# Optimization experiments

Measured on AMD Instinct MI355X. Metric: run time of the kernel, lower is better.

Reference implementation:

```python
import jax, jax.numpy as jnp
import numpy as np

DIM = 512
NUM_HEADS = 16
WS = 8  # window_size
N = WS * WS
B = 1024


def get_relative_index(h, w):
    coords_h = np.arange(h)[:, None].repeat(w, axis=1)
    coords_w = np.arange(w)[None, :].repeat(h, axis=0)
    coords = np.stack([coords_h, coords_w], axis=-1).reshape(-1, 2)  # [N,2]
    rel = coords[:, None, :] - coords[None, :, :]
    rel = rel + np.array([h - 1, w - 1])
    rel[:, :, 0] *= 2 * w - 1
    return rel.sum(-1).astype(np.int32)  # [N,N]


def setup_inputs() -> dict:
    key = jax.random.key(0)
    ks = jax.random.split(key, 6)
    table_size = (2 * WS - 1) * (2 * WS - 1)  # 225
    return {
        "x": jax.random.normal(ks[0], (B, N, DIM), dtype=jnp.float32),
        "qkv_weight": jax.random.normal(ks[1], (3 * DIM, DIM), dtype=jnp.float32) * 0.02,
        "qkv_bias": jax.random.normal(ks[2], (3 * DIM,), dtype=jnp.float32) * 0.02,
        "proj_weight": jax.random.normal(ks[3], (DIM, DIM), dtype=jnp.float32) * 0.02,
        "proj_bias": jax.random.normal(ks[4], (DIM,), dtype=jnp.float32) * 0.02,
        "relative_table": jax.random.normal(ks[5], (table_size, 2 * NUM_HEADS), dtype=jnp.float32) * 0.02,
        "relative_index": jnp.asarray(get_relative_index(WS, WS)),
    }


def reference(x, qkv_weight, qkv_bias, proj_weight, proj_bias, relative_table, relative_index):
    B_, n, C = x.shape
    H = NUM_HEADS
    hd = C // H
    scale = hd ** -0.5
    # qkv projection: [B,N,3C] -> [3,B,H,N,hd]
    qkv = (x @ qkv_weight.T + qkv_bias).reshape(B_, n, 3, H, hd).transpose(2, 0, 3, 1, 4)
    q, k, v = qkv[0], qkv[1], qkv[2]
    attn = jnp.einsum("bhnd,bhmd->bhnm", q * scale, k)  # [B,H,N,N]
    # learned relative-position bias + post-softmax scale
    params = relative_table[relative_index.reshape(-1)].reshape(n, n, 2 * H)
    params = params.transpose(2, 0, 1)  # [2H,N,N]
    rel_bias, rel_scale = params[:H], params[H:]
    attn = jax.nn.softmax(attn + rel_bias[None], axis=-1)
    attn = attn * rel_scale[None]
    out = jnp.einsum("bhnm,bhmd->bhnd", attn, v)
    out = out.transpose(0, 2, 1, 3).reshape(B_, n, C)
    return out @ proj_weight.T + proj_bias
```

## Files before the change

kernel.cpp:

```cpp
#include <hip/hip_runtime.h>

typedef unsigned short u16;
typedef unsigned int   u32;
typedef __attribute__((ext_vector_type(8))) short bf16x8;
typedef __attribute__((ext_vector_type(4))) float f32x4;

#define SCALE 0.17677669529663687f

__device__ __forceinline__ u16 f2bf(float f){
  u32 x = __float_as_uint(f);
  x += 0x7fffu + ((x >> 16) & 1u);
  return (u16)(x >> 16);
}
__device__ __forceinline__ float bf2f(u16 u){
  return __uint_as_float(((u32)u) << 16);
}


__global__ void prep_kernel(const float* __restrict__ qkvw, const float* __restrict__ projw,
                            const float* __restrict__ table, const int* __restrict__ relidx,
                            u16* __restrict__ qkvw_b, u16* __restrict__ projw_b,
                            u16* __restrict__ biasT, u16* __restrict__ scaleT){
  int i = blockIdx.x * 256 + threadIdx.x;
  if (i < 786432) {
    qkvw_b[i] = f2bf(qkvw[i]);
  } else if (i < 1048576) {
    int j = i - 786432; projw_b[j] = f2bf(projw[j]);
  } else if (i < 1114112) {
    int j = i - 1048576; int h = j >> 12, rc = j & 4095;
    int idx = relidx[rc];
    biasT [h*4096 + rc] = f2bf(table[idx*32 + h]);
    scaleT[h*4096 + rc] = f2bf(table[idx*32 + 16 + h]);
  }
}

__global__ void xconv_kernel(const float* __restrict__ x, u16* __restrict__ xb){
  size_t i = (size_t)blockIdx.x * 256 + threadIdx.x;
  const float4* xp = (const float4*)x;
  float4 a = xp[2*i], b = xp[2*i+1];
  union { u16 u[8]; uint4 v; } o;
  o.u[0]=f2bf(a.x); o.u[1]=f2bf(a.y); o.u[2]=f2bf(a.z); o.u[3]=f2bf(a.w);
  o.u[4]=f2bf(b.x); o.u[5]=f2bf(b.y); o.u[6]=f2bf(b.z); o.u[7]=f2bf(b.w);
  *(uint4*)(xb + 8*i) = o.v;
}

template<int EPI>
__global__ __launch_bounds__(512, 2) void gemm_kernel(
    const u16* __restrict__ A, const u16* __restrict__ W,
    const float* __restrict__ bias, void* __restrict__ outp, const int NT)
{
  __shared__ u16 lds[3][16384];
  const int tid = threadIdx.x, lane = tid & 63, wid = tid >> 6;
  const int wave_base = tid & ~63;

  const int cpx = gridDim.x >> 3;
  const int bid = (blockIdx.x & 7) * cpx + (blockIdx.x >> 3);
  const int mt = bid / NT, nt = bid % NT;
  const size_t m0 = (size_t)mt * 256;
  const int n0 = nt * 256;
  const int wm = wid >> 2, wn = wid & 3;

  const f32x4 z = {0.f, 0.f, 0.f, 0.f};
  f32x4 acc[8][4];
#pragma unroll
  for (int i = 0; i < 8; i++)
#pragma unroll
    for (int j = 0; j < 4; j++) acc[i][j] = z;

  auto stageA = [&](int ch){
    const int slot = ch % 3;
    const int kb = ch * 32;
#pragma unroll
    for (int c = 0; c < 2; ++c){
      const int t = c*512 + tid;
      const int row = t >> 2, sl = t & 3;
      const int lsl = sl ^ ((row >> 1) & 3);
      const u16* ga = A + (m0 + row)*512 + kb + lsl*8;
      u16* la = &lds[slot][(size_t)(c*512 + wave_base)*8];
      __builtin_amdgcn_global_load_lds((const __attribute__((address_space(1))) u32*)ga,
                                       (__attribute__((address_space(3))) u32*)la, 16, 0, 0);
    }
  };
  auto stageB = [&](int ch){
    const int slot = ch % 3;
    const int kb = ch * 32;
#pragma unroll
    for (int c = 0; c < 2; ++c){
      const int t = c*512 + tid;
      const int col = t >> 2, sl = t & 3;
      const int lsl = sl ^ ((col >> 1) & 3);
      const u16* gb = W + (size_t)(n0 + col)*512 + kb + lsl*8;
      u16* lb = &lds[slot][8192 + (size_t)(c*512 + wave_base)*8];
      __builtin_amdgcn_global_load_lds((const __attribute__((address_space(1))) u32*)gb,
                                       (__attribute__((address_space(3))) u32*)lb, 16, 0, 0);
    }
  };

  stageA(0); stageB(0);
  stageA(1); stageB(1);
  asm volatile("s_waitcnt vmcnt(4)" ::: "memory");
  __builtin_amdgcn_s_barrier();

  const int lq = lane & 15, lk = lane >> 4;
#pragma unroll
  for (int ch = 0; ch < 16; ++ch){
    const int slot = ch % 3;
    const u16* As = &lds[slot][0];
    const u16* Bs = &lds[slot][8192];
    bf16x8 af[4], bfr[4], af2[4];

#pragma unroll
    for (int i = 0; i < 4; ++i){
      const int row = wm*128 + i*16 + lq;
      af[i]  = *(const bf16x8*)&As[row*32 + (lk ^ ((row >> 1) & 3))*8];
      const int col = wn*64 + i*16 + lq;
      bfr[i] = *(const bf16x8*)&Bs[col*32 + (lk ^ ((col >> 1) & 3))*8];
    }
    if (ch + 2 < 16) stageA(ch + 2);
    __builtin_amdgcn_s_barrier();
    asm volatile("s_waitcnt lgkmcnt(0)" ::: "memory");
    __builtin_amdgcn_sched_barrier(0);
    __builtin_amdgcn_s_setprio(1);
#pragma unroll
    for (int i = 0; i < 4; ++i)
#pragma unroll
      for (int j = 0; j < 4; ++j)
        acc[i][j] = __builtin_amdgcn_mfma_f32_16x16x32_bf16(af[i], bfr[j], acc[i][j], 0, 0, 0);
    __builtin_amdgcn_s_setprio(0);
    __builtin_amdgcn_s_barrier();

#pragma unroll
    for (int i = 0; i < 4; ++i){
      const int row = wm*128 + 64 + i*16 + lq;
      af2[i] = *(const bf16x8*)&As[row*32 + (lk ^ ((row >> 1) & 3))*8];
    }
    if (ch + 2 < 16) stageB(ch + 2);
    __builtin_amdgcn_s_barrier();
    asm volatile("s_waitcnt lgkmcnt(0)" ::: "memory");
    __builtin_amdgcn_sched_barrier(0);
    __builtin_amdgcn_s_setprio(1);
#pragma unroll
    for (int i = 0; i < 4; ++i)
#pragma unroll
      for (int j = 0; j < 4; ++j)
        acc[4+i][j] = __builtin_amdgcn_mfma_f32_16x16x32_bf16(af2[i], bfr[j], acc[4+i][j], 0, 0, 0);
    __builtin_amdgcn_s_setprio(0);
    if (ch < 14)       { asm volatile("s_waitcnt vmcnt(4)" ::: "memory"); }
    else if (ch == 14) { asm volatile("s_waitcnt vmcnt(0)" ::: "memory"); }
    if (ch < 15) __builtin_amdgcn_s_barrier();
  }

  const int lr = (lane >> 4) << 2;
  const int lc = lane & 15;
  if (EPI == 0){
    u16* o = (u16*)outp;
    float bv[4], sc[4];
#pragma unroll
    for (int nf = 0; nf < 4; ++nf){
      const int col = n0 + wn*64 + nf*16 + lc;
      bv[nf] = bias[col];
      sc[nf] = (col < 512) ? SCALE : 1.f;
    }
#pragma unroll
    for (int mf = 0; mf < 8; ++mf){
#pragma unroll
      for (int r = 0; r < 4; ++r){
        const size_t row = m0 + wm*128 + mf*16 + lr + r;
#pragma unroll
        for (int nf = 0; nf < 4; ++nf){
          const int col = n0 + wn*64 + nf*16 + lc;
          o[row*1536 + col] = f2bf((acc[mf][nf][r] + bv[nf]) * sc[nf]);
        }
      }
    }
  } else {
    float* o = (float*)outp;
    float bv[4];
#pragma unroll
    for (int nf = 0; nf < 4; ++nf)
      bv[nf] = bias[n0 + wn*64 + nf*16 + lc];
#pragma unroll
    for (int mf = 0; mf < 8; ++mf){
#pragma unroll
      for (int r = 0; r < 4; ++r){
        const size_t row = m0 + wm*128 + mf*16 + lr + r;
#pragma unroll
        for (int nf = 0; nf < 4; ++nf){
          const int col = n0 + wn*64 + nf*16 + lc;
          o[row*512 + col] = acc[mf][nf][r] + bv[nf];
        }
      }
    }
  }
}

__global__ __launch_bounds__(256) void attn_kernel(
    const u16* __restrict__ qkv, const u16* __restrict__ biasT,
    const u16* __restrict__ scaleT, u16* __restrict__ attn_out)
{
  __shared__ u16 qs[64*40];
  __shared__ u16 ks[64*40];
  __shared__ u16 vs[64*40];
  __shared__ u16 Ps[64*72];
  const int tid = threadIdx.x, lane = tid & 63, wid = tid >> 6;
  const int bh = blockIdx.x, b = bh >> 4, h = bh & 15;
  const u16* base = qkv + (size_t)b * 64 * 1536 + h * 32;
  {
    const int row = tid >> 2, seg = (tid & 3) * 8;
    const size_t ro = (size_t)row * 1536 + seg;
    *(uint4*)&qs[row*40 + seg] = *(const uint4*)(base + ro);
    *(uint4*)&ks[row*40 + seg] = *(const uint4*)(base + ro + 512);
    *(uint4*)&vs[row*40 + seg] = *(const uint4*)(base + ro + 1024);
  }
  __syncthreads();

  const int wr0 = wid * 16;
  const int lg = lane >> 4, lc = lane & 15;
  const f32x4 z = {0.f, 0.f, 0.f, 0.f};

  bf16x8 qf = *(const bf16x8*)&qs[(wr0 + lc)*40 + lg*8];
  f32x4 s[4];
#pragma unroll
  for (int ct = 0; ct < 4; ++ct){
    bf16x8 kf = *(const bf16x8*)&ks[(ct*16 + lc)*40 + lg*8];
    s[ct] = __builtin_amdgcn_mfma_f32_16x16x32_bf16(qf, kf, z, 0, 0, 0);
  }

  const u16* bT = biasT + h*4096;
  const u16* sT = scaleT + h*4096;
#pragma unroll
  for (int r = 0; r < 4; ++r){
    const int row = wr0 + lg*4 + r;
    float vals[4]; float mx = -1e30f;
#pragma unroll
    for (int ct = 0; ct < 4; ++ct){
      vals[ct] = s[ct][r] + bf2f(bT[row*64 + ct*16 + lc]);
      mx = fmaxf(mx, vals[ct]);
    }
    mx = fmaxf(mx, __shfl_xor(mx, 1));
    mx = fmaxf(mx, __shfl_xor(mx, 2));
    mx = fmaxf(mx, __shfl_xor(mx, 4));
    mx = fmaxf(mx, __shfl_xor(mx, 8));
    float sm = 0.f;
#pragma unroll
    for (int ct = 0; ct < 4; ++ct){ vals[ct] = __expf(vals[ct] - mx); sm += vals[ct]; }
    sm += __shfl_xor(sm, 1);
    sm += __shfl_xor(sm, 2);
    sm += __shfl_xor(sm, 4);
    sm += __shfl_xor(sm, 8);
    const float inv = 1.f / sm;
#pragma unroll
    for (int ct = 0; ct < 4; ++ct){
      const int col = ct*16 + lc;
      Ps[row*72 + col] = f2bf(vals[ct] * inv * bf2f(sT[row*64 + col]));
    }
  }
  __syncthreads();

  f32x4 o[2] = {z, z};
#pragma unroll
  for (int kc = 0; kc < 2; ++kc){
    bf16x8 pf = *(const bf16x8*)&Ps[(wr0 + lc)*72 + kc*32 + lg*8];
#pragma unroll
    for (int c2 = 0; c2 < 2; ++c2){
      union { u16 u[8]; bf16x8 v; } vf;
#pragma unroll
      for (int e = 0; e < 8; ++e)
        vf.u[e] = vs[(kc*32 + lg*8 + e)*40 + c2*16 + lc];
      o[c2] = __builtin_amdgcn_mfma_f32_16x16x32_bf16(pf, vf.v, o[c2], 0, 0, 0);
    }
  }

#pragma unroll
  for (int c2 = 0; c2 < 2; ++c2){
#pragma unroll
    for (int r = 0; r < 4; ++r){
      const int n = wr0 + lg*4 + r;
      attn_out[((size_t)b*64 + n)*512 + h*32 + c2*16 + lc] = f2bf(o[c2][r]);
    }
  }
}

extern "C" void kernel_launch(void* const* d_in, const int* in_sizes, int n_in,
                              void* d_out, int out_size, void* d_ws, size_t ws_size,
                              hipStream_t stream)
{
  const float* x      = (const float*)d_in[0];
  const float* qkvw   = (const float*)d_in[1];
  const float* qkvb   = (const float*)d_in[2];
  const float* projw  = (const float*)d_in[3];
  const float* projb  = (const float*)d_in[4];
  const float* table  = (const float*)d_in[5];
  const int*   relidx = (const int*)d_in[6];
  char* ws = (char*)d_ws;

  u16* qkvw_b = (u16*)(ws + 0);
  u16* projw_b= (u16*)(ws + 1572864);
  u16* biasT  = (u16*)(ws + 2097152);
  u16* scaleT = (u16*)(ws + 2228224);
  u16* qkvws  = (u16*)(ws + 2359296);
  u16* xb     = (u16*)(ws + 203685888);
  u16* attn_o = xb;

  if (ws_size < 270794752ull) return;

  prep_kernel<<<dim3(4352), dim3(256), 0, stream>>>(qkvw, projw, table, relidx,
                                                    qkvw_b, projw_b, biasT, scaleT);
  xconv_kernel<<<dim3(16384), dim3(256), 0, stream>>>(x, xb);
  gemm_kernel<0><<<dim3(1536), dim3(512), 0, stream>>>(xb, qkvw_b, qkvb, (void*)qkvws, 6);
  attn_kernel<<<dim3(16384), dim3(256), 0, stream>>>(qkvws, biasT, scaleT, attn_o);
  gemm_kernel<1><<<dim3(512), dim3(512), 0, stream>>>(attn_o, projw_b, projb, d_out, 2);
}
```

Baseline: 287.1 us.

## Shrink GEMM tile to 128x256 and simplify the triple-buffered pipeline

Halves the GEMM M-tile from 256 to 128 rows, cuts accumulators from 8x4 to 4x4 fragments and LDS from 96KB to 72KB, and raises the launch-bounds occupancy hint from 2 to 4 blocks. The A and B loads are merged into one staging call issued at the top of each K chunk, which removes the split half-step with its extra barriers. Grids double so there are more, smaller blocks, aiming for better occupancy and latency hiding. In exchange each block does less MFMA work per byte loaded, since each B tile is now reused over only 128 rows, so global and LDS traffic per flop rises.

```diff
diff --git a/kernel.cpp b/kernel.cpp
--- a/kernel.cpp
+++ b/kernel.cpp
@@ -45,79 +45,71 @@
 }
 
 template<int EPI>
-__global__ __launch_bounds__(512, 2) void gemm_kernel(
+__global__ __launch_bounds__(512, 4) void gemm_kernel(
     const u16* __restrict__ A, const u16* __restrict__ W,
     const float* __restrict__ bias, void* __restrict__ outp, const int NT)
 {
-  __shared__ u16 lds[3][16384];
-  const int tid = threadIdx.x, lane = tid & 63, wid = tid >> 6;
-  const int wave_base = tid & ~63;
+  __shared__ u16 lds[3][12288];
+  const int tid = threadIdx.x, lane = tid & 63;
+  const int wid = tid >> 6, wave_base = tid & ~63;
 
   const int cpx = gridDim.x >> 3;
   const int bid = (blockIdx.x & 7) * cpx + (blockIdx.x >> 3);
   const int mt = bid / NT, nt = bid % NT;
-  const size_t m0 = (size_t)mt * 256;
+  const size_t m0 = (size_t)mt * 128;
   const int n0 = nt * 256;
   const int wm = wid >> 2, wn = wid & 3;
 
   const f32x4 z = {0.f, 0.f, 0.f, 0.f};
-  f32x4 acc[8][4];
-#pragma unroll
-  for (int i = 0; i < 8; i++)
+  f32x4 acc[4][4];
+#pragma unroll
+  for (int i = 0; i < 4; i++)
 #pragma unroll
     for (int j = 0; j < 4; j++) acc[i][j] = z;
 
-  auto stageA = [&](int ch){
+  auto stage = [&](int ch){
     const int slot = ch % 3;
     const int kb = ch * 32;
-#pragma unroll
-    for (int c = 0; c < 2; ++c){
-      const int t = c*512 + tid;
-      const int row = t >> 2, sl = t & 3;
+    {
+      const int row = tid >> 2, sl = tid & 3;
       const int lsl = sl ^ ((row >> 1) & 3);
       const u16* ga = A + (m0 + row)*512 + kb + lsl*8;
-      u16* la = &lds[slot][(size_t)(c*512 + wave_base)*8];
+      u16* la = &lds[slot][(size_t)wave_base*8];
       __builtin_amdgcn_global_load_lds((const __attribute__((address_space(1))) u32*)ga,
                                        (__attribute__((address_space(3))) u32*)la, 16, 0, 0);
     }
-  };
-  auto stageB = [&](int ch){
-    const int slot = ch % 3;
-    const int kb = ch * 32;
 #pragma unroll
     for (int c = 0; c < 2; ++c){
       const int t = c*512 + tid;
       const int col = t >> 2, sl = t & 3;
       const int lsl = sl ^ ((col >> 1) & 3);
       const u16* gb = W + (size_t)(n0 + col)*512 + kb + lsl*8;
-      u16* lb = &lds[slot][8192 + (size_t)(c*512 + wave_base)*8];
+      u16* lb = &lds[slot][4096 + (size_t)(c*512 + wave_base)*8];
       __builtin_amdgcn_global_load_lds((const __attribute__((address_space(1))) u32*)gb,
                                        (__attribute__((address_space(3))) u32*)lb, 16, 0, 0);
     }
   };
 
-  stageA(0); stageB(0);
-  stageA(1); stageB(1);
-  asm volatile("s_waitcnt vmcnt(4)" ::: "memory");
+  stage(0);
+  stage(1);
+  asm volatile("s_waitcnt vmcnt(3)" ::: "memory");
   __builtin_amdgcn_s_barrier();
 
   const int lq = lane & 15, lk = lane >> 4;
 #pragma unroll
   for (int ch = 0; ch < 16; ++ch){
     const int slot = ch % 3;
+    if (ch + 2 < 16) stage(ch + 2);
     const u16* As = &lds[slot][0];
-    const u16* Bs = &lds[slot][8192];
-    bf16x8 af[4], bfr[4], af2[4];
-
+    const u16* Bs = &lds[slot][4096];
+    bf16x8 af[4], bfr[4];
 #pragma unroll
     for (int i = 0; i < 4; ++i){
-      const int row = wm*128 + i*16 + lq;
+      const int row = wm*64 + i*16 + lq;
       af[i]  = *(const bf16x8*)&As[row*32 + (lk ^ ((row >> 1) & 3))*8];
       const int col = wn*64 + i*16 + lq;
       bfr[i] = *(const bf16x8*)&Bs[col*32 + (lk ^ ((col >> 1) & 3))*8];
     }
-    if (ch + 2 < 16) stageA(ch + 2);
-    __builtin_amdgcn_s_barrier();
     asm volatile("s_waitcnt lgkmcnt(0)" ::: "memory");
     __builtin_amdgcn_sched_barrier(0);
     __builtin_amdgcn_s_setprio(1);
@@ -127,25 +119,7 @@
       for (int j = 0; j < 4; ++j)
         acc[i][j] = __builtin_amdgcn_mfma_f32_16x16x32_bf16(af[i], bfr[j], acc[i][j], 0, 0, 0);
     __builtin_amdgcn_s_setprio(0);
-    __builtin_amdgcn_s_barrier();
-
-#pragma unroll
-    for (int i = 0; i < 4; ++i){
-      const int row = wm*128 + 64 + i*16 + lq;
-      af2[i] = *(const bf16x8*)&As[row*32 + (lk ^ ((row >> 1) & 3))*8];
-    }
-    if (ch + 2 < 16) stageB(ch + 2);
-    __builtin_amdgcn_s_barrier();
-    asm volatile("s_waitcnt lgkmcnt(0)" ::: "memory");
-    __builtin_amdgcn_sched_barrier(0);
-    __builtin_amdgcn_s_setprio(1);
-#pragma unroll
-    for (int i = 0; i < 4; ++i)
-#pragma unroll
-      for (int j = 0; j < 4; ++j)
-        acc[4+i][j] = __builtin_amdgcn_mfma_f32_16x16x32_bf16(af2[i], bfr[j], acc[4+i][j], 0, 0, 0);
-    __builtin_amdgcn_s_setprio(0);
-    if (ch < 14)       { asm volatile("s_waitcnt vmcnt(4)" ::: "memory"); }
+    if (ch <= 13)      { asm volatile("s_waitcnt vmcnt(3)" ::: "memory"); }
     else if (ch == 14) { asm volatile("s_waitcnt vmcnt(0)" ::: "memory"); }
     if (ch < 15) __builtin_amdgcn_s_barrier();
   }
@@ -162,10 +136,10 @@
       sc[nf] = (col < 512) ? SCALE : 1.f;
     }
 #pragma unroll
-    for (int mf = 0; mf < 8; ++mf){
+    for (int mf = 0; mf < 4; ++mf){
 #pragma unroll
       for (int r = 0; r < 4; ++r){
-        const size_t row = m0 + wm*128 + mf*16 + lr + r;
+        const size_t row = m0 + wm*64 + mf*16 + lr + r;
 #pragma unroll
         for (int nf = 0; nf < 4; ++nf){
           const int col = n0 + wn*64 + nf*16 + lc;
@@ -180,10 +154,10 @@
     for (int nf = 0; nf < 4; ++nf)
       bv[nf] = bias[n0 + wn*64 + nf*16 + lc];
 #pragma unroll
-    for (int mf = 0; mf < 8; ++mf){
+    for (int mf = 0; mf < 4; ++mf){
 #pragma unroll
       for (int r = 0; r < 4; ++r){
-        const size_t row = m0 + wm*128 + mf*16 + lr + r;
+        const size_t row = m0 + wm*64 + mf*16 + lr + r;
 #pragma unroll
         for (int nf = 0; nf < 4; ++nf){
           const int col = n0 + wn*64 + nf*16 + lc;
@@ -307,7 +281,7 @@
   prep_kernel<<<dim3(4352), dim3(256), 0, stream>>>(qkvw, projw, table, relidx,
                                                     qkvw_b, projw_b, biasT, scaleT);
   xconv_kernel<<<dim3(16384), dim3(256), 0, stream>>>(x, xb);
-  gemm_kernel<0><<<dim3(1536), dim3(512), 0, stream>>>(xb, qkvw_b, qkvb, (void*)qkvws, 6);
+  gemm_kernel<0><<<dim3(3072), dim3(512), 0, stream>>>(xb, qkvw_b, qkvb, (void*)qkvws, 6);
   attn_kernel<<<dim3(16384), dim3(256), 0, stream>>>(qkvws, biasT, scaleT, attn_o);
-  gemm_kernel<1><<<dim3(512), dim3(512), 0, stream>>>(attn_o, projw_b, projb, d_out, 2);
-}
+  gemm_kernel<1><<<dim3(1024), dim3(512), 0, stream>>>(attn_o, projw_b, projb, d_out, 2);
+}
```

Measured after the change: 296.4 us. 3.3% more time.

## Fuse window attention with output projection into one per-window kernel

Applied to the files above, without the earlier changes.

Replaces the per-(window,head) attention kernel and the separate projection GEMM with one kernel per window. Each wave handles two heads, writes its attention output into a swizzled LDS tile, then all waves run the 64x512x512 projection reading weights straight from global memory. This removes the bf16 attention-output round trip through HBM and one launch. The bias and scale tables are also re-laid out so each lane reads four values with one vector load. The cost is lower parallelism (1024 blocks), heavy LDS use per block, and projection weights fetched from global/L2 by every block with no LDS staging.

```diff
diff --git a/kernel.cpp b/kernel.cpp
--- a/kernel.cpp
+++ b/kernel.cpp
@@ -29,8 +29,10 @@
   } else if (i < 1114112) {
     int j = i - 1048576; int h = j >> 12, rc = j & 4095;
     int idx = relidx[rc];
-    biasT [h*4096 + rc] = f2bf(table[idx*32 + h]);
-    scaleT[h*4096 + rc] = f2bf(table[idx*32 + 16 + h]);
+    int row = rc >> 6, col = rc & 63;
+    int noff = h*4096 + row*64 + (col & 15)*4 + (col >> 4);
+    biasT [noff] = f2bf(table[idx*32 + h]);
+    scaleT[noff] = f2bf(table[idx*32 + 16 + h]);
   }
 }
 
@@ -44,10 +46,9 @@
   *(uint4*)(xb + 8*i) = o.v;
 }
 
-template<int EPI>
-__global__ __launch_bounds__(512, 2) void gemm_kernel(
+__global__ __launch_bounds__(512, 2) void gemm_qkv_kernel(
     const u16* __restrict__ A, const u16* __restrict__ W,
-    const float* __restrict__ bias, void* __restrict__ outp, const int NT)
+    const float* __restrict__ bias, u16* __restrict__ outp)
 {
   __shared__ u16 lds[3][16384];
   const int tid = threadIdx.x, lane = tid & 63, wid = tid >> 6;
@@ -55,7 +56,7 @@
 
   const int cpx = gridDim.x >> 3;
   const int bid = (blockIdx.x & 7) * cpx + (blockIdx.x >> 3);
-  const int mt = bid / NT, nt = bid % NT;
+  const int mt = bid / 6, nt = bid % 6;
   const size_t m0 = (size_t)mt * 256;
   const int n0 = nt * 256;
   const int wm = wid >> 2, wn = wid & 3;
@@ -152,131 +153,170 @@
 
   const int lr = (lane >> 4) << 2;
   const int lc = lane & 15;
-  if (EPI == 0){
-    u16* o = (u16*)outp;
-    float bv[4], sc[4];
-#pragma unroll
-    for (int nf = 0; nf < 4; ++nf){
-      const int col = n0 + wn*64 + nf*16 + lc;
-      bv[nf] = bias[col];
-      sc[nf] = (col < 512) ? SCALE : 1.f;
-    }
-#pragma unroll
-    for (int mf = 0; mf < 8; ++mf){
+  u16* o = outp;
+  float bv[4], sc[4];
+#pragma unroll
+  for (int nf = 0; nf < 4; ++nf){
+    const int col = n0 + wn*64 + nf*16 + lc;
+    bv[nf] = bias[col];
+    sc[nf] = (col < 512) ? SCALE : 1.f;
+  }
+#pragma unroll
+  for (int mf = 0; mf < 8; ++mf){
+#pragma unroll
+    for (int r = 0; r < 4; ++r){
+      const size_t row = m0 + wm*128 + mf*16 + lr + r;
+#pragma unroll
+      for (int nf = 0; nf < 4; ++nf){
+        const int col = n0 + wn*64 + nf*16 + lc;
+        o[row*1536 + col] = f2bf((acc[mf][nf][r] + bv[nf]) * sc[nf]);
+      }
+    }
+  }
+}
+
+__global__ __launch_bounds__(512) void attnproj_kernel(
+    const u16* __restrict__ qkv, const u16* __restrict__ biasT,
+    const u16* __restrict__ scaleT, const u16* __restrict__ projw,
+    const float* __restrict__ projb, float* __restrict__ out)
+{
+  __shared__ u16 lds[62464];
+  const int tid = threadIdx.x, lane = tid & 63, wid = tid >> 6;
+  const int lq = lane & 15, lg = lane >> 4;
+  const int b = blockIdx.x;
+  const u16* qb = qkv + (size_t)b * 64 * 1536;
+  u16* vs = &lds[32768 + wid*3712];
+  u16* Ps = vs + 2560;
+  const f32x4 z = {0.f, 0.f, 0.f, 0.f};
+
+#pragma unroll
+  for (int hh = 0; hh < 2; ++hh){
+    const int h = wid*2 + hh;
+    asm volatile("s_waitcnt lgkmcnt(0)" ::: "memory");
+    __builtin_amdgcn_sched_barrier(0);
+#pragma unroll
+    for (int c = 0; c < 4; ++c){
+      const int u = c*64 + lane, row = u >> 2, sg = u & 3;
+      uint4 t = *(const uint4*)(qb + row*1536 + 1024 + h*32 + sg*8);
+      *(uint4*)&vs[row*40 + sg*8] = t;
+    }
+    bf16x8 qf[4], kf[4];
+#pragma unroll
+    for (int i = 0; i < 4; ++i){
+      qf[i] = *(const bf16x8*)(qb + (i*16+lq)*1536 + h*32 + lg*8);
+      kf[i] = *(const bf16x8*)(qb + (i*16+lq)*1536 + 512 + h*32 + lg*8);
+    }
+    f32x4 s[4][4];
+#pragma unroll
+    for (int i = 0; i < 4; ++i)
+#pragma unroll
+      for (int j = 0; j < 4; ++j)
+        s[i][j] = __builtin_amdgcn_mfma_f32_16x16x32_bf16(qf[i], kf[j], z, 0, 0, 0);
+
+    const u16* bT = biasT + h*4096;
+    const u16* sT = scaleT + h*4096;
+    f32x4 o[4][2];
+#pragma unroll
+    for (int i = 0; i < 4; ++i){ o[i][0] = z; o[i][1] = z; }
+
+#pragma unroll
+    for (int i = 0; i < 4; ++i){
 #pragma unroll
       for (int r = 0; r < 4; ++r){
-        const size_t row = m0 + wm*128 + mf*16 + lr + r;
-#pragma unroll
-        for (int nf = 0; nf < 4; ++nf){
-          const int col = n0 + wn*64 + nf*16 + lc;
-          o[row*1536 + col] = f2bf((acc[mf][nf][r] + bv[nf]) * sc[nf]);
+        const int row = i*16 + lg*4 + r;
+        const ushort4 b4 = *(const ushort4*)&bT[row*64 + lq*4];
+        const ushort4 s4 = *(const ushort4*)&sT[row*64 + lq*4];
+        float vals[4];
+        vals[0] = s[i][0][r] + bf2f(b4.x);
+        vals[1] = s[i][1][r] + bf2f(b4.y);
+        vals[2] = s[i][2][r] + bf2f(b4.z);
+        vals[3] = s[i][3][r] + bf2f(b4.w);
+        float mx = fmaxf(fmaxf(vals[0], vals[1]), fmaxf(vals[2], vals[3]));
+        mx = fmaxf(mx, __shfl_xor(mx, 1));
+        mx = fmaxf(mx, __shfl_xor(mx, 2));
+        mx = fmaxf(mx, __shfl_xor(mx, 4));
+        mx = fmaxf(mx, __shfl_xor(mx, 8));
+        float sm = 0.f;
+#pragma unroll
+        for (int j = 0; j < 4; ++j){ vals[j] = __expf(vals[j] - mx); sm += vals[j]; }
+        sm += __shfl_xor(sm, 1);
+        sm += __shfl_xor(sm, 2);
+        sm += __shfl_xor(sm, 4);
+        sm += __shfl_xor(sm, 8);
+        const float inv = 1.f / sm;
+        const u16 sv[4] = {s4.x, s4.y, s4.z, s4.w};
+#pragma unroll
+        for (int j = 0; j < 4; ++j)
+          Ps[(lg*4 + r)*72 + j*16 + lq] = f2bf(vals[j] * inv * bf2f(sv[j]));
+      }
+      asm volatile("s_waitcnt lgkmcnt(0)" ::: "memory");
+      __builtin_amdgcn_sched_barrier(0);
+#pragma unroll
+      for (int kc = 0; kc < 2; ++kc){
+        bf16x8 pa = *(const bf16x8*)&Ps[lq*72 + kc*32 + lg*8];
+#pragma unroll
+        for (int c2 = 0; c2 < 2; ++c2){
+          union { u16 u[8]; bf16x8 v; } vf;
+#pragma unroll
+          for (int e = 0; e < 8; ++e)
+            vf.u[e] = vs[(kc*32 + lg*8 + e)*40 + c2*16 + lq];
+          o[i][c2] = __builtin_amdgcn_mfma_f32_16x16x32_bf16(pa, vf.v, o[i][c2], 0, 0, 0);
         }
       }
     }
-  } else {
-    float* o = (float*)outp;
-    float bv[4];
-#pragma unroll
-    for (int nf = 0; nf < 4; ++nf)
-      bv[nf] = bias[n0 + wn*64 + nf*16 + lc];
-#pragma unroll
-    for (int mf = 0; mf < 8; ++mf){
-#pragma unroll
-      for (int r = 0; r < 4; ++r){
-        const size_t row = m0 + wm*128 + mf*16 + lr + r;
-#pragma unroll
-        for (int nf = 0; nf < 4; ++nf){
-          const int col = n0 + wn*64 + nf*16 + lc;
-          o[row*512 + col] = acc[mf][nf][r] + bv[nf];
+#pragma unroll
+    for (int i = 0; i < 4; ++i){
+#pragma unroll
+      for (int c2 = 0; c2 < 2; ++c2){
+#pragma unroll
+        for (int r = 0; r < 4; ++r){
+          const int row = i*16 + lg*4 + r;
+          const int c = h*32 + c2*16 + lq;
+          const int phys = (c >> 3) ^ (row & 7);
+          lds[row*512 + phys*8 + (c & 7)] = f2bf(o[i][c2][r]);
         }
       }
     }
   }
-}
-
-__global__ __launch_bounds__(256) void attn_kernel(
-    const u16* __restrict__ qkv, const u16* __restrict__ biasT,
-    const u16* __restrict__ scaleT, u16* __restrict__ attn_out)
-{
-  __shared__ u16 qs[64*40];
-  __shared__ u16 ks[64*40];
-  __shared__ u16 vs[64*40];
-  __shared__ u16 Ps[64*72];
-  const int tid = threadIdx.x, lane = tid & 63, wid = tid >> 6;
-  const int bh = blockIdx.x, b = bh >> 4, h = bh & 15;
-  const u16* base = qkv + (size_t)b * 64 * 1536 + h * 32;
-  {
-    const int row = tid >> 2, seg = (tid & 3) * 8;
-    const size_t ro = (size_t)row * 1536 + seg;
-    *(uint4*)&qs[row*40 + seg] = *(const uint4*)(base + ro);
-    *(uint4*)&ks[row*40 + seg] = *(const uint4*)(base + ro + 512);
-    *(uint4*)&vs[row*40 + seg] = *(const uint4*)(base + ro + 1024);
-  }
   __syncthreads();
 
-  const int wr0 = wid * 16;
-  const int lg = lane >> 4, lc = lane & 15;
-  const f32x4 z = {0.f, 0.f, 0.f, 0.f};
-
-  bf16x8 qf = *(const bf16x8*)&qs[(wr0 + lc)*40 + lg*8];
-  f32x4 s[4];
-#pragma unroll
-  for (int ct = 0; ct < 4; ++ct){
-    bf16x8 kf = *(const bf16x8*)&ks[(ct*16 + lc)*40 + lg*8];
-    s[ct] = __builtin_amdgcn_mfma_f32_16x16x32_bf16(qf, kf, z, 0, 0, 0);
-  }
-
-  const u16* bT = biasT + h*4096;
-  const u16* sT = scaleT + h*4096;
-#pragma unroll
-  for (int r = 0; r < 4; ++r){
-    const int row = wr0 + lg*4 + r;
-    float vals[4]; float mx = -1e30f;
-#pragma unroll
-    for (int ct = 0; ct < 4; ++ct){
-      vals[ct] = s[ct][r] + bf2f(bT[row*64 + ct*16 + lc]);
-      mx = fmaxf(mx, vals[ct]);
-    }
-    mx = fmaxf(mx, __shfl_xor(mx, 1));
-    mx = fmaxf(mx, __shfl_xor(mx, 2));
-    mx = fmaxf(mx, __shfl_xor(mx, 4));
-    mx = fmaxf(mx, __shfl_xor(mx, 8));
-    float sm = 0.f;
-#pragma unroll
-    for (int ct = 0; ct < 4; ++ct){ vals[ct] = __expf(vals[ct] - mx); sm += vals[ct]; }
-    sm += __shfl_xor(sm, 1);
-    sm += __shfl_xor(sm, 2);
-    sm += __shfl_xor(sm, 4);
-    sm += __shfl_xor(sm, 8);
-    const float inv = 1.f / sm;
-#pragma unroll
-    for (int ct = 0; ct < 4; ++ct){
-      const int col = ct*16 + lc;
-      Ps[row*72 + col] = f2bf(vals[ct] * inv * bf2f(sT[row*64 + col]));
-    }
-  }
-  __syncthreads();
-
-  f32x4 o[2] = {z, z};
-#pragma unroll
-  for (int kc = 0; kc < 2; ++kc){
-    bf16x8 pf = *(const bf16x8*)&Ps[(wr0 + lc)*72 + kc*32 + lg*8];
-#pragma unroll
-    for (int c2 = 0; c2 < 2; ++c2){
-      union { u16 u[8]; bf16x8 v; } vf;
-#pragma unroll
-      for (int e = 0; e < 8; ++e)
-        vf.u[e] = vs[(kc*32 + lg*8 + e)*40 + c2*16 + lc];
-      o[c2] = __builtin_amdgcn_mfma_f32_16x16x32_bf16(pf, vf.v, o[c2], 0, 0, 0);
-    }
-  }
-
-#pragma unroll
-  for (int c2 = 0; c2 < 2; ++c2){
+  const int n0 = wid * 64;
+  f32x4 pacc[4][4];
+#pragma unroll
+  for (int i = 0; i < 4; i++)
+#pragma unroll
+    for (int j = 0; j < 4; j++) pacc[i][j] = z;
+
+#pragma unroll
+  for (int ch = 0; ch < 16; ++ch){
+    bf16x8 oa[4], wb[4];
+#pragma unroll
+    for (int mi = 0; mi < 4; ++mi){
+      const int row = mi*16 + lq;
+      const int phys = (ch*4 + lg) ^ (lq & 7);
+      oa[mi] = *(const bf16x8*)&lds[row*512 + phys*8];
+    }
+#pragma unroll
+    for (int nj = 0; nj < 4; ++nj)
+      wb[nj] = *(const bf16x8*)(projw + (size_t)(n0 + nj*16 + lq)*512 + ch*32 + lg*8);
+#pragma unroll
+    for (int mi = 0; mi < 4; ++mi)
+#pragma unroll
+      for (int nj = 0; nj < 4; ++nj)
+        pacc[mi][nj] = __builtin_amdgcn_mfma_f32_16x16x32_bf16(oa[mi], wb[nj], pacc[mi][nj], 0, 0, 0);
+  }
+
+  float bv[4];
+#pragma unroll
+  for (int nj = 0; nj < 4; ++nj) bv[nj] = projb[n0 + nj*16 + lq];
+#pragma unroll
+  for (int mi = 0; mi < 4; ++mi){
 #pragma unroll
     for (int r = 0; r < 4; ++r){
-      const int n = wr0 + lg*4 + r;
-      attn_out[((size_t)b*64 + n)*512 + h*32 + c2*16 + lc] = f2bf(o[c2][r]);
+      const size_t grow = (size_t)b*64 + mi*16 + lg*4 + r;
+#pragma unroll
+      for (int nj = 0; nj < 4; ++nj)
+        out[grow*512 + n0 + nj*16 + lq] = pacc[mi][nj][r] + bv[nj];
     }
   }
 }
@@ -300,14 +340,13 @@
   u16* scaleT = (u16*)(ws + 2228224);
   u16* qkvws  = (u16*)(ws + 2359296);
   u16* xb     = (u16*)(ws + 203685888);
-  u16* attn_o = xb;
 
   if (ws_size < 270794752ull) return;
 
   prep_kernel<<<dim3(4352), dim3(256), 0, stream>>>(qkvw, projw, table, relidx,
                                                     qkvw_b, projw_b, biasT, scaleT);
   xconv_kernel<<<dim3(16384), dim3(256), 0, stream>>>(x, xb);
-  gemm_kernel<0><<<dim3(1536), dim3(512), 0, stream>>>(xb, qkvw_b, qkvb, (void*)qkvws, 6);
-  attn_kernel<<<dim3(16384), dim3(256), 0, stream>>>(qkvws, biasT, scaleT, attn_o);
-  gemm_kernel<1><<<dim3(512), dim3(512), 0, stream>>>(attn_o, projw_b, projb, d_out, 2);
-}
+  gemm_qkv_kernel<<<dim3(1536), dim3(512), 0, stream>>>(xb, qkvw_b, qkvb, qkvws);
+  attnproj_kernel<<<dim3(1024), dim3(512), 0, stream>>>(qkvws, biasT, scaleT,
+                                                        projw_b, projb, (float*)d_out);
+}
```

Measured after the change: 344.9 us. 20.1% more time.

## Process two heads per attention block with register-prefetched second head

Applied to the files above, without the earlier changes.

Each attention block now handles two heads of the same window. The second head's Q/K/V loads are issued into registers before the first head is computed, then stored to a second LDS buffer. The relative bias/scale tables are re-laid out in prep so each lane can fetch its four values with one vector load instead of four scalar loads. The LDS barrier between writing P and reading it is replaced by a waitcnt plus sched_barrier, which relies on each wave reading only the P rows it wrote itself. In exchange there are half as many blocks, and the extra buffers raise LDS and register use.

```diff
diff --git a/kernel.cpp b/kernel.cpp
--- a/kernel.cpp
+++ b/kernel.cpp
@@ -29,8 +29,10 @@
   } else if (i < 1114112) {
     int j = i - 1048576; int h = j >> 12, rc = j & 4095;
     int idx = relidx[rc];
-    biasT [h*4096 + rc] = f2bf(table[idx*32 + h]);
-    scaleT[h*4096 + rc] = f2bf(table[idx*32 + 16 + h]);
+    int row = rc >> 6, col = rc & 63;
+    int noff = h*4096 + row*64 + (col & 15)*4 + (col >> 4);
+    biasT [noff] = f2bf(table[idx*32 + h]);
+    scaleT[noff] = f2bf(table[idx*32 + 16 + h]);
   }
 }
 
@@ -198,87 +200,102 @@
     const u16* __restrict__ qkv, const u16* __restrict__ biasT,
     const u16* __restrict__ scaleT, u16* __restrict__ attn_out)
 {
-  __shared__ u16 qs[64*40];
-  __shared__ u16 ks[64*40];
-  __shared__ u16 vs[64*40];
-  __shared__ u16 Ps[64*72];
+  __shared__ u16 qs[2][2560];
+  __shared__ u16 ks[2][2560];
+  __shared__ u16 vs[2][2560];
+  __shared__ u16 Ps[4608];
   const int tid = threadIdx.x, lane = tid & 63, wid = tid >> 6;
-  const int bh = blockIdx.x, b = bh >> 4, h = bh & 15;
-  const u16* base = qkv + (size_t)b * 64 * 1536 + h * 32;
-  {
-    const int row = tid >> 2, seg = (tid & 3) * 8;
-    const size_t ro = (size_t)row * 1536 + seg;
-    *(uint4*)&qs[row*40 + seg] = *(const uint4*)(base + ro);
-    *(uint4*)&ks[row*40 + seg] = *(const uint4*)(base + ro + 512);
-    *(uint4*)&vs[row*40 + seg] = *(const uint4*)(base + ro + 1024);
-  }
+  const int lq = lane & 15, lg = lane >> 4;
+  const int row = tid >> 2, sg = (tid & 3) * 8;
+  const int b  = blockIdx.x >> 3;
+  const int h0 = (blockIdx.x & 7) * 2;
+  const u16* pbase = qkv + ((size_t)b*64 + row)*1536 + sg;
+  const int wr0 = wid * 16;
+  const f32x4 z = {0.f, 0.f, 0.f, 0.f};
+
+  auto compute = [&](int buf, int h){
+    bf16x8 qf = *(const bf16x8*)&qs[buf][(wr0 + lq)*40 + lg*8];
+    f32x4 s[4];
+#pragma unroll
+    for (int ct = 0; ct < 4; ++ct){
+      bf16x8 kf = *(const bf16x8*)&ks[buf][(ct*16 + lq)*40 + lg*8];
+      s[ct] = __builtin_amdgcn_mfma_f32_16x16x32_bf16(qf, kf, z, 0, 0, 0);
+    }
+    const u16* bT = biasT + h*4096;
+    const u16* sT = scaleT + h*4096;
+#pragma unroll
+    for (int r = 0; r < 4; ++r){
+      const int rq = wr0 + lg*4 + r;
+      const ushort4 b4 = *(const ushort4*)&bT[rq*64 + lq*4];
+      const ushort4 s4 = *(const ushort4*)&sT[rq*64 + lq*4];
+      float vals[4];
+      vals[0] = s[0][r] + bf2f(b4.x);
+      vals[1] = s[1][r] + bf2f(b4.y);
+      vals[2] = s[2][r] + bf2f(b4.z);
+      vals[3] = s[3][r] + bf2f(b4.w);
+      float mx = fmaxf(fmaxf(vals[0], vals[1]), fmaxf(vals[2], vals[3]));
+      mx = fmaxf(mx, __shfl_xor(mx, 1));
+      mx = fmaxf(mx, __shfl_xor(mx, 2));
+      mx = fmaxf(mx, __shfl_xor(mx, 4));
+      mx = fmaxf(mx, __shfl_xor(mx, 8));
+      float sm = 0.f;
+#pragma unroll
+      for (int j = 0; j < 4; ++j){ vals[j] = __expf(vals[j] - mx); sm += vals[j]; }
+      sm += __shfl_xor(sm, 1);
+      sm += __shfl_xor(sm, 2);
+      sm += __shfl_xor(sm, 4);
+      sm += __shfl_xor(sm, 8);
+      const float inv = 1.f / sm;
+      const u16 sv[4] = {s4.x, s4.y, s4.z, s4.w};
+#pragma unroll
+      for (int j = 0; j < 4; ++j)
+        Ps[rq*72 + j*16 + lq] = f2bf(vals[j] * inv * bf2f(sv[j]));
+    }
+    asm volatile("s_waitcnt lgkmcnt(0)" ::: "memory");
+    __builtin_amdgcn_sched_barrier(0);
+
+    f32x4 o[2] = {z, z};
+#pragma unroll
+    for (int kc = 0; kc < 2; ++kc){
+      bf16x8 pa = *(const bf16x8*)&Ps[(wr0 + lq)*72 + kc*32 + lg*8];
+#pragma unroll
+      for (int c2 = 0; c2 < 2; ++c2){
+        union { u16 u[8]; bf16x8 v; } vf;
+#pragma unroll
+        for (int e = 0; e < 8; ++e)
+          vf.u[e] = vs[buf][(kc*32 + lg*8 + e)*40 + c2*16 + lq];
+        o[c2] = __builtin_amdgcn_mfma_f32_16x16x32_bf16(pa, vf.v, o[c2], 0, 0, 0);
+      }
+    }
+#pragma unroll
+    for (int c2 = 0; c2 < 2; ++c2){
+#pragma unroll
+      for (int r = 0; r < 4; ++r){
+        const int n = wr0 + lg*4 + r;
+        attn_out[((size_t)b*64 + n)*512 + h*32 + c2*16 + lq] = f2bf(o[c2][r]);
+      }
+    }
+  };
+
+  uint4 q0 = *(const uint4*)(pbase + h0*32);
+  uint4 k0 = *(const uint4*)(pbase + 512 + h0*32);
+  uint4 v0 = *(const uint4*)(pbase + 1024 + h0*32);
+  *(uint4*)&qs[0][row*40 + sg] = q0;
+  *(uint4*)&ks[0][row*40 + sg] = k0;
+  *(uint4*)&vs[0][row*40 + sg] = v0;
+  uint4 q1 = *(const uint4*)(pbase + (h0+1)*32);
+  uint4 k1 = *(const uint4*)(pbase + 512 + (h0+1)*32);
+  uint4 v1 = *(const uint4*)(pbase + 1024 + (h0+1)*32);
   __syncthreads();
 
-  const int wr0 = wid * 16;
-  const int lg = lane >> 4, lc = lane & 15;
-  const f32x4 z = {0.f, 0.f, 0.f, 0.f};
-
-  bf16x8 qf = *(const bf16x8*)&qs[(wr0 + lc)*40 + lg*8];
-  f32x4 s[4];
-#pragma unroll
-  for (int ct = 0; ct < 4; ++ct){
-    bf16x8 kf = *(const bf16x8*)&ks[(ct*16 + lc)*40 + lg*8];
-    s[ct] = __builtin_amdgcn_mfma_f32_16x16x32_bf16(qf, kf, z, 0, 0, 0);
-  }
-
-  const u16* bT = biasT + h*4096;
-  const u16* sT = scaleT + h*4096;
-#pragma unroll
-  for (int r = 0; r < 4; ++r){
-    const int row = wr0 + lg*4 + r;
-    float vals[4]; float mx = -1e30f;
-#pragma unroll
-    for (int ct = 0; ct < 4; ++ct){
-      vals[ct] = s[ct][r] + bf2f(bT[row*64 + ct*16 + lc]);
-      mx = fmaxf(mx, vals[ct]);
-    }
-    mx = fmaxf(mx, __shfl_xor(mx, 1));
-    mx = fmaxf(mx, __shfl_xor(mx, 2));
-    mx = fmaxf(mx, __shfl_xor(mx, 4));
-    mx = fmaxf(mx, __shfl_xor(mx, 8));
-    float sm = 0.f;
-#pragma unroll
-    for (int ct = 0; ct < 4; ++ct){ vals[ct] = __expf(vals[ct] - mx); sm += vals[ct]; }
-    sm += __shfl_xor(sm, 1);
-    sm += __shfl_xor(sm, 2);
-    sm += __shfl_xor(sm, 4);
-    sm += __shfl_xor(sm, 8);
-    const float inv = 1.f / sm;
-#pragma unroll
-    for (int ct = 0; ct < 4; ++ct){
-      const int col = ct*16 + lc;
-      Ps[row*72 + col] = f2bf(vals[ct] * inv * bf2f(sT[row*64 + col]));
-    }
-  }
+  compute(0, h0);
+
+  *(uint4*)&qs[1][row*40 + sg] = q1;
+  *(uint4*)&ks[1][row*40 + sg] = k1;
+  *(uint4*)&vs[1][row*40 + sg] = v1;
   __syncthreads();
 
-  f32x4 o[2] = {z, z};
-#pragma unroll
-  for (int kc = 0; kc < 2; ++kc){
-    bf16x8 pf = *(const bf16x8*)&Ps[(wr0 + lc)*72 + kc*32 + lg*8];
-#pragma unroll
-    for (int c2 = 0; c2 < 2; ++c2){
-      union { u16 u[8]; bf16x8 v; } vf;
-#pragma unroll
-      for (int e = 0; e < 8; ++e)
-        vf.u[e] = vs[(kc*32 + lg*8 + e)*40 + c2*16 + lc];
-      o[c2] = __builtin_amdgcn_mfma_f32_16x16x32_bf16(pf, vf.v, o[c2], 0, 0, 0);
-    }
-  }
-
-#pragma unroll
-  for (int c2 = 0; c2 < 2; ++c2){
-#pragma unroll
-    for (int r = 0; r < 4; ++r){
-      const int n = wr0 + lg*4 + r;
-      attn_out[((size_t)b*64 + n)*512 + h*32 + c2*16 + lc] = f2bf(o[c2][r]);
-    }
-  }
+  compute(1, h0 + 1);
 }
 
 extern "C" void kernel_launch(void* const* d_in, const int* in_sizes, int n_in,
@@ -308,6 +325,6 @@
                                                     qkvw_b, projw_b, biasT, scaleT);
   xconv_kernel<<<dim3(16384), dim3(256), 0, stream>>>(x, xb);
   gemm_kernel<0><<<dim3(1536), dim3(512), 0, stream>>>(xb, qkvw_b, qkvb, (void*)qkvws, 6);
-  attn_kernel<<<dim3(16384), dim3(256), 0, stream>>>(qkvws, biasT, scaleT, attn_o);
+  attn_kernel<<<dim3(8192), dim3(256), 0, stream>>>(qkvws, biasT, scaleT, attn_o);
   gemm_kernel<1><<<dim3(512), dim3(512), 0, stream>>>(attn_o, projw_b, projb, d_out, 2);
 }
```

After: 284.1 us. About the same (-1.0%).
